# Performance work log

Hardware: AMD Instinct MI355X
Metric: run time of the kernel (lower is better)

The kernel has to match this reference:

```python
import jax, jax.numpy as jnp
import numpy as np

BN_EPS = 1e-5


def _bn_relu(x, gamma, beta):
    # BatchNorm1d in train mode over (batch, spatial) per channel, then ReLU.
    mean = jnp.mean(x, axis=(0, 2), keepdims=True)
    var = jnp.var(x, axis=(0, 2), keepdims=True)
    xn = (x - mean) * jax.lax.rsqrt(var + BN_EPS)
    return jax.nn.relu(xn * gamma[None, :, None] + beta[None, :, None])


def setup_inputs() -> dict:
    key = jax.random.key(0)
    ks = jax.random.split(key, 12)
    B, d1, d2, n_p, n_g = 16, 128, 256, 8192, 2048
    d_cat, d_h, d_out = d1 + d2, 256, 128
    return {
        "feature1": jax.random.normal(ks[0], (B, d1, n_p), jnp.float32),
        "coord1": jax.random.normal(ks[1], (B, 3, n_p), jnp.float32),
        "feature2": jax.random.normal(ks[2], (B, d2, n_g), jnp.float32),
        "coord2": jax.random.normal(ks[3], (B, 3, n_g), jnp.float32),
        "W1": jax.random.normal(ks[4], (d_h, d_cat), jnp.float32) * 0.05,
        "b1": jax.random.normal(ks[5], (d_h,), jnp.float32) * 0.05,
        "gamma1": jnp.ones((d_h,), jnp.float32),
        "beta1": jnp.zeros((d_h,), jnp.float32),
        "W2": jax.random.normal(ks[6], (d_out, d_h), jnp.float32) * 0.05,
        "b2": jax.random.normal(ks[7], (d_out,), jnp.float32) * 0.05,
        "gamma2": jnp.ones((d_out,), jnp.float32),
        "beta2": jnp.zeros((d_out,), jnp.float32),
    }


def reference(feature1, coord1, feature2, coord2,
              W1, b1, gamma1, beta1, W2, b2, gamma2, beta2):
    c1 = coord1.transpose(0, 2, 1)      # [B, n_p, 3]
    c2 = coord2.transpose(0, 2, 1)      # [B, n_g, 3]
    f2 = feature2.transpose(0, 2, 1)    # [B, n_g, d2]

    # squared pairwise distances [B, n_p, n_g]
    d2sq = (jnp.sum(c1 * c1, -1)[:, :, None]
            + jnp.sum(c2 * c2, -1)[:, None, :]
            - 2.0 * jnp.einsum('bpd,bgd->bpg', c1, c2))

    # 3 nearest neighbors via top_k of negated distances (ascending distance)
    neg, idx = jax.lax.top_k(-d2sq, 3)
    dists = -neg                                     # [B, n_p, 3]
    recip = 1.0 / (dists + 1e-8)
    weight = recip / jnp.sum(recip, axis=-1, keepdims=True)

    gathered = jax.vmap(lambda f, i: f[i])(f2, idx)  # [B, n_p, 3, d2]
    interp = jnp.sum(gathered * weight[..., None], axis=2)  # [B, n_p, d2]

    feat = jnp.concatenate([feature1.transpose(0, 2, 1), interp], axis=-1)
    feat = feat.transpose(0, 2, 1)                   # [B, d1+d2, n_p]

    h = _bn_relu(jnp.einsum('oc,bcn->bon', W1, feat) + b1[None, :, None], gamma1, beta1)
    out = _bn_relu(jnp.einsum('oc,bcn->bon', W2, h) + b2[None, :, None], gamma2, beta2)
    return out
```

## Files before the change

### kernel.cpp

```cpp
#include <hip/hip_runtime.h>

#define BB   16
#define D1   128
#define D2   256
#define NP   8192
#define NG   2048
#define DC   384
#define DH   256
#define DO   128
#define NPTS (BB*NP)
#define KRANGE 4
#define KSLICE (NG/KRANGE)

typedef unsigned int u32;
typedef unsigned short u16;
typedef short v8s __attribute__((ext_vector_type(8)));
typedef float v4f __attribute__((ext_vector_type(4)));

__device__ __forceinline__ u16 f2bf(float f) {
  u32 u = __builtin_bit_cast(u32, f);
  return (u16)((u + 0x7FFFu + ((u >> 16) & 1u)) >> 16);
}
__device__ __forceinline__ float bf2f(u32 lo16) {
  return __builtin_bit_cast(float, lo16 << 16);
}

__device__ __forceinline__ void gload16(const void* g, void* s) {
  __builtin_amdgcn_global_load_lds((const __attribute__((address_space(1))) void*)g,
                                   (__attribute__((address_space(3))) void*)s, 16, 0, 0);
}

__global__ __launch_bounds__(256) void prepw_kernel(const float* __restrict__ W1,
                                                    const float* __restrict__ W2,
                                                    u16* __restrict__ W1s, u16* __restrict__ W2s) {
  int id = blockIdx.x * 256 + threadIdx.x;
  if (id < 12288) {
    int ks = id >> 11, rem = id & 2047, m = rem >> 3, blk = rem & 7;
    int k = ks * 64 + (blk ^ (m & 7)) * 8;
    const float* src = W1 + m * 384 + k;
    u32 a0 = (u32)f2bf(src[0]) | ((u32)f2bf(src[1]) << 16);
    u32 a1 = (u32)f2bf(src[2]) | ((u32)f2bf(src[3]) << 16);
    u32 a2 = (u32)f2bf(src[4]) | ((u32)f2bf(src[5]) << 16);
    u32 a3 = (u32)f2bf(src[6]) | ((u32)f2bf(src[7]) << 16);
    uint4 v; v.x=a0; v.y=a1; v.z=a2; v.w=a3;
    *(uint4*)((char*)W1s + (long)id * 16) = v;
  }
  int id2 = id - 12288;
  if (id2 >= 0 && id2 < 4096) {
    int ks = id2 >> 10, rem = id2 & 1023, m = rem >> 3, blk = rem & 7;
    int k = ks * 64 + (blk ^ (m & 7)) * 8;
    const float* src = W2 + m * 256 + k;
    u32 a0 = (u32)f2bf(src[0]) | ((u32)f2bf(src[1]) << 16);
    u32 a1 = (u32)f2bf(src[2]) | ((u32)f2bf(src[3]) << 16);
    u32 a2 = (u32)f2bf(src[4]) | ((u32)f2bf(src[5]) << 16);
    u32 a3 = (u32)f2bf(src[6]) | ((u32)f2bf(src[7]) << 16);
    uint4 v; v.x=a0; v.y=a1; v.z=a2; v.w=a3;
    *(uint4*)((char*)W2s + (long)id2 * 16) = v;
  }
}

__global__ __launch_bounds__(256) void tf2_kernel(const float* __restrict__ f2, u16* __restrict__ f2t) {
  __shared__ float tl[64 * 65];
  int b = blockIdx.z, t = threadIdx.x;
  int c0 = blockIdx.y * 64, g0 = blockIdx.x * 64;
  const float* src = f2 + ((long)b * 256 + c0) * 2048 + g0;
  for (int i = t; i < 4096; i += 256) {
    int c = i >> 6, g = i & 63;
    tl[c * 65 + g] = src[(long)c * 2048 + g];
  }
  __syncthreads();
  for (int i = t; i < 2048; i += 256) {
    int g = i >> 5, cp = i & 31;
    int c = cp * 2;
    u32 v = (u32)f2bf(tl[c * 65 + g]) | ((u32)f2bf(tl[(c + 1) * 65 + g]) << 16);
    *(u32*)((char*)f2t + (((long)b * 2048 + g0 + g) * 256 + c0 + c) * 2) = v;
  }
}

__global__ __launch_bounds__(256) void knn_part_kernel(const float* __restrict__ c1, const float* __restrict__ c2,
                                                       float* __restrict__ ktD, int* __restrict__ ktI, int rbase) {
  __shared__ float4 sg[KSLICE];
  int b = blockIdx.z, r = rbase + blockIdx.y, t = threadIdx.x;
  int base = r * KSLICE;
  const float* c2b = c2 + (long)b * 3 * NG;
  for (int g = t; g < KSLICE; g += 256) {
    int gg = base + g;
    float x = c2b[gg], y = c2b[NG + gg], z = c2b[2 * NG + gg];
    float s2 = __fadd_rn(__fadd_rn(__fmul_rn(x, x), __fmul_rn(y, y)), __fmul_rn(z, z));
    sg[g] = make_float4(x, y, z, s2);
  }
  __syncthreads();
  int p = blockIdx.x * 256 + t;
  const float* c1b = c1 + (long)b * 3 * NP;
  float px = c1b[p], py = c1b[NP + p], pz = c1b[2 * NP + p];
  float s1 = __fadd_rn(__fadd_rn(__fmul_rn(px, px), __fmul_rn(py, py)), __fmul_rn(pz, pz));
  float t0 = 1e30f, t1 = 1e30f, t2v = 1e30f;
  int i0 = 0, i1 = 0, i2 = 0;
  for (int g0 = 0; g0 < KSLICE; g0 += 8) {
    u32 mask = 0;
    #pragma unroll
    for (int u = 0; u < 8; u++) {
      float4 q = sg[g0 + u];
      float dot = __fadd_rn(__fadd_rn(__fmul_rn(px, q.x), __fmul_rn(py, q.y)), __fmul_rn(pz, q.z));
      float du = __fsub_rn(__fadd_rn(s1, q.w), __fmul_rn(2.0f, dot));
      mask |= (du < t2v) ? (1u << u) : 0u;
    }
    while (mask) {
      int u = __builtin_ctz(mask);
      mask &= mask - 1;
      float4 q = sg[g0 + u];
      float dot = __fadd_rn(__fadd_rn(__fmul_rn(px, q.x), __fmul_rn(py, q.y)), __fmul_rn(pz, q.z));
      float dd = __fsub_rn(__fadd_rn(s1, q.w), __fmul_rn(2.0f, dot));
      int gi = base + g0 + u;
      bool c0 = dd < t0, cc1 = dd < t1, cc2 = dd < t2v;
      int ni2 = cc1 ? i1 : (cc2 ? gi : i2);
      int ni1 = c0 ? i0 : (cc1 ? gi : i1);
      int ni0 = c0 ? gi : i0;
      float nt2 = __builtin_amdgcn_fmed3f(t1, dd, t2v);
      float nt1 = __builtin_amdgcn_fmed3f(t0, dd, t1);
      float nt0 = fminf(t0, dd);
      t0 = nt0; t1 = nt1; t2v = nt2;
      i0 = ni0; i1 = ni1; i2 = ni2;
    }
  }
  long n = (long)b * NP + p;
  long o = (long)(r * 3) * NPTS + n;
  ktD[o] = t0; ktD[o + NPTS] = t1; ktD[o + 2 * (long)NPTS] = t2v;
  ktI[o] = i0; ktI[o + NPTS] = i1; ktI[o + 2 * (long)NPTS] = i2;
}

__global__ __launch_bounds__(256) void interp_kernel(const float* __restrict__ f1, const u16* __restrict__ f2t,
                                                     const float* __restrict__ ktD, const int* __restrict__ ktI,
                                                     u16* __restrict__ feat) {
  __shared__ float tile[32 * 129];
  int b = blockIdx.y, t = threadIdx.x;
  long p0 = (long)blockIdx.x * 32;
  const float* f1b = f1 + (long)b * D1 * NP;
  #pragma unroll
  for (int k = 0; k < 16; k++) {
    int i = k * 256 + t;
    int c = i >> 5, p = i & 31;
    tile[p * 129 + c] = f1b[(long)c * NP + p0 + p];
  }
  __syncthreads();
  int p = t >> 3, q = t & 7;
  long n = (long)b * NP + p0 + p;
  char* row = (char*)feat + n * 768;
  int sw = p & 7;
  #pragma unroll
  for (int g = 0; g < 2; g++) {
    int c = g * 64 + q * 8;
    const float* tp = tile + p * 129 + c;
    u32 w0 = (u32)f2bf(tp[0]) | ((u32)f2bf(tp[1]) << 16);
    u32 w1 = (u32)f2bf(tp[2]) | ((u32)f2bf(tp[3]) << 16);
    u32 w2 = (u32)f2bf(tp[4]) | ((u32)f2bf(tp[5]) << 16);
    u32 w3 = (u32)f2bf(tp[6]) | ((u32)f2bf(tp[7]) << 16);
    uint4 v; v.x=w0; v.y=w1; v.z=w2; v.w=w3;
    *(uint4*)(row + g * 128 + ((q ^ sw) << 4)) = v;
  }
  float t0 = 1e30f, t1 = 1e30f, t2v = 1e30f;
  int i0 = 0, i1 = 0, i2 = 0;
  #pragma unroll
  for (int e = 0; e < KRANGE * 3; e++) {
    float d = ktD[(long)e * NPTS + n];
    int gi = ktI[(long)e * NPTS + n];
    if (d < t2v) {
      if (d < t1) {
        t2v = t1; i2 = i1;
        if (d < t0) { t1 = t0; i1 = i0; t0 = d; i0 = gi; }
        else        { t1 = d;  i1 = gi; }
      } else { t2v = d; i2 = gi; }
    }
  }
  float rr0 = __fdiv_rn(1.0f, __fadd_rn(t0, 1e-8f));
  float rr1 = __fdiv_rn(1.0f, __fadd_rn(t1, 1e-8f));
  float rr2 = __fdiv_rn(1.0f, __fadd_rn(t2v, 1e-8f));
  float rs = __fadd_rn(__fadd_rn(rr0, rr1), rr2);
  float w0 = __fdiv_rn(rr0, rs);
  float w1 = __fdiv_rn(rr1, rs);
  float w2 = __fdiv_rn(rr2, rs);
  const char* fb = (const char*)f2t + (long)b * NG * 512;
  const char* r0 = fb + (long)i0 * 512;
  const char* r1 = fb + (long)i1 * 512;
  const char* r2 = fb + (long)i2 * 512;
  #pragma unroll
  for (int g = 0; g < 4; g++) {
    int ci = g * 64 + q * 8;
    uint4 a0 = *(const uint4*)(r0 + ci * 2);
    uint4 a1 = *(const uint4*)(r1 + ci * 2);
    uint4 a2 = *(const uint4*)(r2 + ci * 2);
    const u32* pa0 = (const u32*)&a0;
    const u32* pa1 = (const u32*)&a1;
    const u32* pa2 = (const u32*)&a2;
    u32 outw[4];
    #pragma unroll
    for (int h = 0; h < 4; h++) {
      u32 x0 = pa0[h], x1 = pa1[h], x2 = pa2[h];
      float lo = w0 * bf2f(x0 & 0xffff) + w1 * bf2f(x1 & 0xffff) + w2 * bf2f(x2 & 0xffff);
      float hi = w0 * bf2f(x0 >> 16)    + w1 * bf2f(x1 >> 16)    + w2 * bf2f(x2 >> 16);
      outw[h] = (u32)f2bf(lo) | ((u32)f2bf(hi) << 16);
    }
    uint4 v; v.x=outw[0]; v.y=outw[1]; v.z=outw[2]; v.w=outw[3];
    *(uint4*)(row + (2 + g) * 128 + ((q ^ sw) << 4)) = v;
  }
}

__device__ __forceinline__ void mfma_tile(const char* lds, int buf, int wm, int wn, int l, v4f acc[4][4]) {
  const char* A = lds + buf * 16384;
  const char* Bp = lds + 32768 + buf * 16384;
  int lm = l & 15, lk = l >> 4, l7 = l & 7;
  #pragma unroll
  for (int w32 = 0; w32 < 2; w32++) {
    v8s af[4], bfr[4];
    #pragma unroll
    for (int mf = 0; mf < 4; mf++)
      af[mf] = *(const v8s*)(A + (wm * 64 + mf * 16 + lm) * 128 + (((w32 * 4 + lk) ^ l7) << 4));
    #pragma unroll
    for (int nf = 0; nf < 4; nf++)
      bfr[nf] = *(const v8s*)(Bp + (wn * 64 + nf * 16 + lm) * 128 + (((w32 * 4 + lk) ^ l7) << 4));
    #pragma unroll
    for (int mf = 0; mf < 4; mf++)
      #pragma unroll
      for (int nf = 0; nf < 4; nf++)
        acc[mf][nf] = __builtin_amdgcn_mfma_f32_16x16x32_bf16(af[mf], bfr[nf], acc[mf][nf], 0, 0, 0);
  }
}

__global__ __launch_bounds__(256) void gemm1_kernel(const u16* __restrict__ W1s, const u16* __restrict__ feat,
                                                    const float* __restrict__ b1, u16* __restrict__ y1,
                                                    float* __restrict__ ps, float* __restrict__ pq) {
  __shared__ __attribute__((aligned(16))) char lds[65536];
  const int t = threadIdx.x, w = t >> 6, l = t & 63;
  const int wm = w >> 1, wn = w & 1;
  const int nb = blockIdx.y, mb = blockIdx.x;
  const long n0 = (long)nb * 128;
  const int m0 = mb * 128;
  v4f acc[4][4];
  #pragma unroll
  for (int i = 0; i < 4; i++)
    #pragma unroll
    for (int j = 0; j < 4; j++) { v4f z = {0.f,0.f,0.f,0.f}; acc[i][j] = z; }

  auto stage = [&](int ks, int buf) {
    const char* srcA = (const char*)W1s + ks * 32768 + (long)m0 * 128 + w * 4096 + l * 16;
    char* dstA = (char*)lds + buf * 16384 + w * 4096;
    #pragma unroll
    for (int i = 0; i < 4; i++) gload16(srcA + i * 1024, dstA + i * 1024);
    char* dstB = (char*)lds + 32768 + buf * 16384 + w * 4096;
    #pragma unroll
    for (int i = 0; i < 4; i++) {
      int a = w * 4096 + i * 1024 + l * 16;
      int n = a >> 7, r = a & 127;
      const char* srcB = (const char*)feat + (n0 + n) * 768 + ks * 128 + r;
      gload16(srcB, dstB + i * 1024);
    }
  };

  stage(0, 0);
  __syncthreads();
  int buf = 0;
  for (int ks = 0; ks < 6; ks++) {
    if (ks < 5) stage(ks + 1, buf ^ 1);
    mfma_tile(lds, buf, wm, wn, l, acc);
    __syncthreads();
    buf ^= 1;
  }

  const int lm = l & 15, lk = l >> 4;
  #pragma unroll
  for (int mf = 0; mf < 4; mf++) {
    int m = m0 + wm * 64 + mf * 16 + lk * 4;
    float bb0 = b1[m], bb1 = b1[m+1], bb2 = b1[m+2], bb3 = b1[m+3];
    #pragma unroll
    for (int nf = 0; nf < 4; nf++) {
      long n = n0 + wn * 64 + nf * 16 + lm;
      v4f v = acc[mf][nf];
      v[0] += bb0; v[1] += bb1; v[2] += bb2; v[3] += bb3;
      acc[mf][nf] = v;
      uint2 pk;
      pk.x = (u32)f2bf(v[0]) | ((u32)f2bf(v[1]) << 16);
      pk.y = (u32)f2bf(v[2]) | ((u32)f2bf(v[3]) << 16);
      *(uint2*)((char*)y1 + (n * 256 + m) * 2) = pk;
    }
  }
  #pragma unroll
  for (int mf = 0; mf < 4; mf++) {
    #pragma unroll
    for (int j = 0; j < 4; j++) {
      float s = 0.f, q = 0.f;
      #pragma unroll
      for (int nf = 0; nf < 4; nf++) { float v = acc[mf][nf][j]; s += v; q += v * v; }
      #pragma unroll
      for (int mask = 1; mask <= 8; mask <<= 1) { s += __shfl_xor(s, mask); q += __shfl_xor(q, mask); }
      if (lm == 0) {
        int m = m0 + wm * 64 + mf * 16 + lk * 4 + j;
        int col = nb * 2 + wn;
        ps[(long)m * 2048 + col] = s;
        pq[(long)m * 2048 + col] = q;
      }
    }
  }
}

__global__ __launch_bounds__(256) void stats_kernel(const float* __restrict__ ps, const float* __restrict__ pq,
                                                    const float* __restrict__ gamma, const float* __restrict__ beta,
                                                    float* __restrict__ scsh, int ncols, float invN) {
  int m = blockIdx.x, t = threadIdx.x;
  float s = 0.f, q = 0.f;
  for (int i = t; i < ncols; i += 256) { s += ps[(long)m * ncols + i]; q += pq[(long)m * ncols + i]; }
  __shared__ float rs[4], rq[4];
  #pragma unroll
  for (int mask = 1; mask <= 32; mask <<= 1) { s += __shfl_xor(s, mask); q += __shfl_xor(q, mask); }
  int w = t >> 6;
  if ((t & 63) == 0) { rs[w] = s; rq[w] = q; }
  __syncthreads();
  if (t == 0) {
    s = rs[0] + rs[1] + rs[2] + rs[3];
    q = rq[0] + rq[1] + rq[2] + rq[3];
    float mean = s * invN;
    float var = q * invN - mean * mean;
    float rstd = rsqrtf(var + 1e-5f);
    float sc = gamma[m] * rstd;
    scsh[m] = sc;
    scsh[gridDim.x + m] = beta[m] - mean * sc;
  }
}

__global__ __launch_bounds__(256) void gemm2_kernel(const u16* __restrict__ W2s, const u16* __restrict__ y1,
                                                    const float* __restrict__ scsh, const float* __restrict__ b2,
                                                    u16* __restrict__ y2, float* __restrict__ ps, float* __restrict__ pq) {
  __shared__ __attribute__((aligned(16))) char lds[65536];
  const int t = threadIdx.x, w = t >> 6, l = t & 63;
  const int wm = w >> 1, wn = w & 1;
  const int nb = blockIdx.x;
  const long n0 = (long)nb * 128;
  v4f acc[4][4];
  #pragma unroll
  for (int i = 0; i < 4; i++)
    #pragma unroll
    for (int j = 0; j < 4; j++) { v4f z = {0.f,0.f,0.f,0.f}; acc[i][j] = z; }
  uint4 breg[4];

  auto stageA = [&](int ks, int buf) {
    const char* src = (const char*)W2s + ks * 16384 + w * 4096 + l * 16;
    char* dst = (char*)lds + buf * 16384 + w * 4096;
    #pragma unroll
    for (int i = 0; i < 4; i++) gload16(src + i * 1024, dst + i * 1024);
  };
  auto loadB = [&](int ks) {
    #pragma unroll
    for (int i = 0; i < 4; i++) {
      int idx = i * 256 + t, n = idx >> 3, blk = idx & 7;
      breg[i] = *(const uint4*)((const char*)y1 + (n0 + n) * 512 + ks * 128 + blk * 16);
    }
  };
  auto writeB = [&](int ks, int buf) {
    #pragma unroll
    for (int i = 0; i < 4; i++) {
      int idx = i * 256 + t, n = idx >> 3, blk = idx & 7;
      const u32* pr = (const u32*)&breg[i];
      u32 outw[4];
      #pragma unroll
      for (int h = 0; h < 4; h++) {
        int k = ks * 64 + blk * 8 + 2 * h;
        u32 x = pr[h];
        float h0 = fmaxf(0.f, scsh[k]     * bf2f(x & 0xffff) + scsh[256 + k]);
        float h1 = fmaxf(0.f, scsh[k + 1] * bf2f(x >> 16)    + scsh[256 + k + 1]);
        outw[h] = (u32)f2bf(h0) | ((u32)f2bf(h1) << 16);
      }
      uint4 v; v.x=outw[0]; v.y=outw[1]; v.z=outw[2]; v.w=outw[3];
      *(uint4*)((char*)lds + 32768 + buf * 16384 + n * 128 + ((blk ^ (n & 7)) << 4)) = v;
    }
  };

  stageA(0, 0); loadB(0); writeB(0, 0);
  __syncthreads();
  int buf = 0;
  for (int ks = 0; ks < 4; ks++) {
    if (ks < 3) { stageA(ks + 1, buf ^ 1); loadB(ks + 1); }
    mfma_tile(lds, buf, wm, wn, l, acc);
    if (ks < 3) writeB(ks + 1, buf ^ 1);
    __syncthreads();
    buf ^= 1;
  }

  const int lm = l & 15, lk = l >> 4;
  #pragma unroll
  for (int mf = 0; mf < 4; mf++) {
    int m = wm * 64 + mf * 16 + lk * 4;
    float bb0 = b2[m], bb1 = b2[m+1], bb2v = b2[m+2], bb3 = b2[m+3];
    #pragma unroll
    for (int nf = 0; nf < 4; nf++) {
      long n = n0 + wn * 64 + nf * 16 + lm;
      v4f v = acc[mf][nf];
      v[0] += bb0; v[1] += bb1; v[2] += bb2v; v[3] += bb3;
      acc[mf][nf] = v;
      uint2 pk;
      pk.x = (u32)f2bf(v[0]) | ((u32)f2bf(v[1]) << 16);
      pk.y = (u32)f2bf(v[2]) | ((u32)f2bf(v[3]) << 16);
      *(uint2*)((char*)y2 + (n * 128 + m) * 2) = pk;
    }
  }
  #pragma unroll
  for (int mf = 0; mf < 4; mf++) {
    #pragma unroll
    for (int j = 0; j < 4; j++) {
      float s = 0.f, q = 0.f;
      #pragma unroll
      for (int nf = 0; nf < 4; nf++) { float v = acc[mf][nf][j]; s += v; q += v * v; }
      #pragma unroll
      for (int mask = 1; mask <= 8; mask <<= 1) { s += __shfl_xor(s, mask); q += __shfl_xor(q, mask); }
      if (lm == 0) {
        int m = wm * 64 + mf * 16 + lk * 4 + j;
        int col = nb * 2 + wn;
        ps[(long)m * 2048 + col] = s;
        pq[(long)m * 2048 + col] = q;
      }
    }
  }
}

__global__ __launch_bounds__(256) void final_kernel(const u16* __restrict__ y2, const float* __restrict__ scsh2,
                                                    float* __restrict__ out) {
  __shared__ float tl[64 * 130];
  __shared__ float sc[128], sh[128];
  int b = blockIdx.y, t = threadIdx.x;
  long p0 = (long)blockIdx.x * 64;
  if (t < 128) { sc[t] = scsh2[t]; sh[t] = scsh2[128 + t]; }
  __syncthreads();
  #pragma unroll
  for (int i = 0; i < 4; i++) {
    int idx = i * 256 + t;
    int n = idx >> 4, cb = idx & 15;
    uint4 v = *(const uint4*)((const char*)y2 + (((long)b * NP + p0 + n) * 128 + cb * 8) * 2);
    const u32* pv = (const u32*)&v;
    #pragma unroll
    for (int h = 0; h < 4; h++) {
      int m = cb * 8 + 2 * h;
      u32 x = pv[h];
      tl[n * 130 + m]     = fmaxf(0.f, sc[m]     * bf2f(x & 0xffff) + sh[m]);
      tl[n * 130 + m + 1] = fmaxf(0.f, sc[m + 1] * bf2f(x >> 16)    + sh[m + 1]);
    }
  }
  __syncthreads();
  int m = t & 127, hh = t >> 7;
  float* dst = out + ((long)b * 128 + m) * NP + p0 + hh * 32;
  #pragma unroll
  for (int j = 0; j < 8; j++) {
    int p = hh * 32 + j * 4;
    float4 v;
    v.x = tl[(p + 0) * 130 + m];
    v.y = tl[(p + 1) * 130 + m];
    v.z = tl[(p + 2) * 130 + m];
    v.w = tl[(p + 3) * 130 + m];
    *(float4*)(dst + j * 4) = v;
  }
}

extern "C" void kernel_launch(void* const* d_in, const int* in_sizes, int n_in,
                              void* d_out, int out_size, void* d_ws, size_t ws_size,
                              hipStream_t stream) {
  const float* f1  = (const float*)d_in[0];
  const float* c1  = (const float*)d_in[1];
  const float* f2  = (const float*)d_in[2];
  const float* c2  = (const float*)d_in[3];
  const float* W1  = (const float*)d_in[4];
  const float* b1  = (const float*)d_in[5];
  const float* g1  = (const float*)d_in[6];
  const float* be1 = (const float*)d_in[7];
  const float* W2  = (const float*)d_in[8];
  const float* b2  = (const float*)d_in[9];
  const float* g2  = (const float*)d_in[10];
  const float* be2 = (const float*)d_in[11];
  float* out = (float*)d_out;

  char* ws = (char*)d_ws;
  size_t off = 0;
  auto alloc = [&](size_t sz) { char* p = ws + off; off = (off + sz + 255) & ~(size_t)255; return p; };
  u16*   f2t   = (u16*)  alloc((size_t)BB * NG * D2 * 2);
  u16*   W1s   = (u16*)  alloc(196608);
  u16*   W2s   = (u16*)  alloc(65536);
  float* ps1   = (float*)alloc((size_t)256 * 2048 * 4);
  float* pq1   = (float*)alloc((size_t)256 * 2048 * 4);
  float* scsh1 = (float*)alloc(2048);
  float* ps2   = (float*)alloc((size_t)128 * 2048 * 4);
  float* pq2   = (float*)alloc((size_t)128 * 2048 * 4);
  float* scsh2 = (float*)alloc(1024);
  u16*   y1    = (u16*)  alloc((size_t)NPTS * DH * 2);
  u16*   feat  = (u16*)  alloc((size_t)NPTS * DC * 2);
  u16*   y2    = (u16*)  feat;

  float* ktD = (float*)y1;
  int*   ktI = (int*)((char*)y1 + (size_t)KRANGE * 3 * NPTS * 4 + 256);

  hipLaunchKernelGGL(prepw_kernel, dim3(64), dim3(256), 0, stream, W1, W2, W1s, W2s);
  hipLaunchKernelGGL(tf2_kernel, dim3(NG / 64, D2 / 64, BB), dim3(256), 0, stream, f2, f2t);
  hipLaunchKernelGGL(knn_part_kernel, dim3(NP / 256, 2, BB), dim3(256), 0, stream, c1, c2, ktD, ktI, 0);
  hipLaunchKernelGGL(knn_part_kernel, dim3(NP / 256, 2, BB), dim3(256), 0, stream, c1, c2, ktD, ktI, 2);
  hipLaunchKernelGGL(interp_kernel, dim3(NP / 32, BB), dim3(256), 0, stream, f1, f2t, ktD, ktI, feat);
  hipLaunchKernelGGL(gemm1_kernel, dim3(2, NPTS / 128), dim3(256), 0, stream, W1s, feat, b1, y1, ps1, pq1);
  hipLaunchKernelGGL(stats_kernel, dim3(256), dim3(256), 0, stream, ps1, pq1, g1, be1, scsh1, 2048, 1.f / (float)NPTS);
  hipLaunchKernelGGL(gemm2_kernel, dim3(NPTS / 128), dim3(256), 0, stream, W2s, y1, scsh1, b2, y2, ps2, pq2);
  hipLaunchKernelGGL(stats_kernel, dim3(128), dim3(256), 0, stream, ps2, pq2, g2, be2, scsh2, 2048, 1.f / (float)NPTS);
  hipLaunchKernelGGL(final_kernel, dim3(NP / 64, BB), dim3(256), 0, stream, y2, scsh2, out);
}
```

Measured before the change: 323.6 us.

## Load GEMM1 MFMA operands directly from global memory, dropping LDS staging

The GEMM1 kernel no longer stages W1 and feature tiles through double-buffered LDS with block barriers. Each wave now reads its MFMA fragments straight from global memory with the same XOR-swizzled k offsets, and launch bounds are set to request three blocks per CU. This removes LDS traffic and __syncthreads, but fragments shared across waves are re-read from global/L2 and the loads are no longer overlapped with compute. Rows of feat are read with a 768-byte stride, which may coalesce worse.

New measurement: 343.6 us. +6.2%, slower.

```diff
diff --git a/kernel.cpp b/kernel.cpp
--- a/kernel.cpp
+++ b/kernel.cpp
@@ -226,47 +226,46 @@
   }
 }
 
-__global__ __launch_bounds__(256) void gemm1_kernel(const u16* __restrict__ W1s, const u16* __restrict__ feat,
-                                                    const float* __restrict__ b1, u16* __restrict__ y1,
-                                                    float* __restrict__ ps, float* __restrict__ pq) {
-  __shared__ __attribute__((aligned(16))) char lds[65536];
+__global__ __launch_bounds__(256, 3) void gemm1_kernel(const u16* __restrict__ W1s, const u16* __restrict__ feat,
+                                                       const float* __restrict__ b1, u16* __restrict__ y1,
+                                                       float* __restrict__ ps, float* __restrict__ pq) {
   const int t = threadIdx.x, w = t >> 6, l = t & 63;
   const int wm = w >> 1, wn = w & 1;
   const int nb = blockIdx.y, mb = blockIdx.x;
   const long n0 = (long)nb * 128;
   const int m0 = mb * 128;
+  const int lm = l & 15, lk = l >> 4, l7 = l & 7;
   v4f acc[4][4];
   #pragma unroll
   for (int i = 0; i < 4; i++)
     #pragma unroll
     for (int j = 0; j < 4; j++) { v4f z = {0.f,0.f,0.f,0.f}; acc[i][j] = z; }
 
-  auto stage = [&](int ks, int buf) {
-    const char* srcA = (const char*)W1s + ks * 32768 + (long)m0 * 128 + w * 4096 + l * 16;
-    char* dstA = (char*)lds + buf * 16384 + w * 4096;
-    #pragma unroll
-    for (int i = 0; i < 4; i++) gload16(srcA + i * 1024, dstA + i * 1024);
-    char* dstB = (char*)lds + 32768 + buf * 16384 + w * 4096;
-    #pragma unroll
-    for (int i = 0; i < 4; i++) {
-      int a = w * 4096 + i * 1024 + l * 16;
-      int n = a >> 7, r = a & 127;
-      const char* srcB = (const char*)feat + (n0 + n) * 768 + ks * 128 + r;
-      gload16(srcB, dstB + i * 1024);
-    }
-  };
-
-  stage(0, 0);
-  __syncthreads();
-  int buf = 0;
+  const char* arow[4];
+  const char* brow[4];
+  #pragma unroll
+  for (int mf = 0; mf < 4; mf++) arow[mf] = (const char*)W1s + (long)(m0 + wm * 64 + mf * 16 + lm) * 128;
+  #pragma unroll
+  for (int nf = 0; nf < 4; nf++) brow[nf] = (const char*)feat + (n0 + wn * 64 + nf * 16 + lm) * 768;
+
+  #pragma unroll
   for (int ks = 0; ks < 6; ks++) {
-    if (ks < 5) stage(ks + 1, buf ^ 1);
-    mfma_tile(lds, buf, wm, wn, l, acc);
-    __syncthreads();
-    buf ^= 1;
-  }
-
-  const int lm = l & 15, lk = l >> 4;
+    #pragma unroll
+    for (int w32 = 0; w32 < 2; w32++) {
+      int off = ((w32 * 4 + lk) ^ l7) << 4;
+      v8s af[4], bfr[4];
+      #pragma unroll
+      for (int mf = 0; mf < 4; mf++) af[mf] = *(const v8s*)(arow[mf] + ks * 32768 + off);
+      #pragma unroll
+      for (int nf = 0; nf < 4; nf++) bfr[nf] = *(const v8s*)(brow[nf] + ks * 128 + off);
+      #pragma unroll
+      for (int mf = 0; mf < 4; mf++)
+        #pragma unroll
+        for (int nf = 0; nf < 4; nf++)
+          acc[mf][nf] = __builtin_amdgcn_mfma_f32_16x16x32_bf16(af[mf], bfr[nf], acc[mf][nf], 0, 0, 0);
+    }
+  }
+
   #pragma unroll
   for (int mf = 0; mf < 4; mf++) {
     int m = m0 + wm * 64 + mf * 16 + lk * 4;
```
